# Performance work log

Measured on AMD Instinct MI355X. Metric: run time of the kernel, lower is better.

The kernel has to match this reference:

```python
import jax, jax.numpy as jnp
import numpy as np
from jax import lax

K = 4096   # input_size
N = 4096   # output_size
FP8_MAX = 448.0  # float8_e4m3fn max finite value


def setup_inputs() -> dict:
    key = jax.random.key(0)
    kx, kw, kws, kb = jax.random.split(key, 4)
    x = jax.random.normal(kx, (2, 4096, K), dtype=jnp.float32)
    # Quantized weight: sample bf16-scale weights, round to fp8_e4m3fn, store raw bits as uint8 [K, N]
    w_f32 = jax.random.normal(kw, (K, N), dtype=jnp.float32) * 8.0
    w_fp8 = jnp.clip(w_f32, -FP8_MAX, FP8_MAX).astype(jnp.float8_e4m3fn)
    qweight = lax.bitcast_convert_type(w_fp8, jnp.uint8)  # [K, N] uint8
    weight_scale = jax.random.uniform(kws, (N,), dtype=jnp.float32, minval=0.001, maxval=0.02)
    input_scale = jnp.asarray([0.01], dtype=jnp.float32)  # static activation scale [1]
    bias = jax.random.normal(kb, (N,), dtype=jnp.float32) * 0.02
    return {"x": x, "qweight": qweight, "weight_scale": weight_scale,
            "input_scale": input_scale, "bias": bias}


def reference(x, qweight, weight_scale, input_scale, bias):
    # _forward_w8a8_static: quantize activations with static scale, fp8 GEMM via
    # _scaled_mm semantics: out = (x_fp8 @ w_fp8) * input_scale * weight_scale + bias
    target_dtype = x.dtype
    x2 = x.reshape(-1, x.shape[-1]).astype(jnp.bfloat16)          # [M, K] bf16 cast as in torch path
    # static per-tensor activation quantization to fp8_e4m3fn
    xq = jnp.clip(x2.astype(jnp.float32) / input_scale[0], -FP8_MAX, FP8_MAX)
    xq = xq.astype(jnp.float8_e4m3fn).astype(jnp.float32)          # [M, K]
    w = lax.bitcast_convert_type(qweight, jnp.float8_e4m3fn).astype(jnp.float32)  # [K, N]
    acc = jnp.einsum('mk,kn->mn', xq, w)                           # fp32 accumulate
    out = acc * (input_scale[0] * weight_scale) + bias             # fused dequant scale + bias
    return out.reshape(*x.shape[:-1], N).astype(target_dtype)
```

## Files before the change

### kernel.cpp

```cpp
#include <hip/hip_runtime.h>
#include <stdint.h>

typedef float f32x4 __attribute__((ext_vector_type(4)));
typedef int   i32x4 __attribute__((ext_vector_type(4)));
typedef int   i32x8 __attribute__((ext_vector_type(8)));

__device__ __forceinline__ void gld16(const uint8_t* g, uint8_t* l) {
  __builtin_amdgcn_global_load_lds(
      (const __attribute__((address_space(1))) void*)g,
      (__attribute__((address_space(3))) void*)l, 16, 0, 0);
}

__device__ __forceinline__ float bf16_rne(float f) {
  uint32_t u = __float_as_uint(f);
  u = (u + 0x7fffu + ((u >> 16) & 1u)) & 0xffff0000u;
  return __uint_as_float(u);
}

__device__ __forceinline__ float quant_prep(float f, float s) {
  float b = bf16_rne(f);
  float v = b / s;
  return fminf(448.f, fmaxf(-448.f, v));
}

__global__ __launch_bounds__(256) void quant_x(
    const float* __restrict__ x, const float* __restrict__ isp,
    uint32_t* __restrict__ xq, int n4) {
  const float s = isp[0];
  int stride = gridDim.x * blockDim.x;
  for (int i = blockIdx.x * blockDim.x + threadIdx.x; i < n4; i += stride) {
    float4 v = ((const float4*)x)[i];
    float c0 = quant_prep(v.x, s);
    float c1 = quant_prep(v.y, s);
    float c2 = quant_prep(v.z, s);
    float c3 = quant_prep(v.w, s);
    int p = 0;
    p = __builtin_amdgcn_cvt_pk_fp8_f32(c0, c1, p, false);
    p = __builtin_amdgcn_cvt_pk_fp8_f32(c2, c3, p, true);
    xq[i] = (uint32_t)p;
  }
}

__global__ __launch_bounds__(256) void transp_w(
    const int* __restrict__ qw, uint8_t* __restrict__ wt) {
  constexpr int K = 4096, N = 4096;
  __shared__ uint8_t t[64 * 80];
  const int n0 = blockIdx.x * 64, k0 = blockIdx.y * 64;
  const int tid = threadIdx.x;
  const int r = tid >> 2, c = tid & 3;
  const int* src = qw + (size_t)(k0 + r) * N + n0 + c * 16;
  union { uint8_t b[16]; uint4 v; } o;
#pragma unroll
  for (int j = 0; j < 16; ++j) o.b[j] = (uint8_t)src[j];
  *(uint4*)(t + r * 80 + c * 16) = o.v;
  __syncthreads();
#pragma unroll
  for (int j = 0; j < 16; ++j) o.b[j] = t[(c * 16 + j) * 80 + r];
  *(uint4*)(wt + (size_t)(n0 + r) * K + k0 + c * 16) = o.v;
}

__device__ __forceinline__ i32x8 ld_frag(const uint8_t* base, int row, int g) {
  const int s = row & 7;
  const i32x4 lo = *(const i32x4*)(base + row * 128 + (((2 * g)     ^ s) * 16));
  const i32x4 hi = *(const i32x4*)(base + row * 128 + (((2 * g + 1) ^ s) * 16));
  i32x8 r;
  r[0] = lo[0]; r[1] = lo[1]; r[2] = lo[2]; r[3] = lo[3];
  r[4] = hi[0]; r[5] = hi[1]; r[6] = hi[2]; r[7] = hi[3];
  return r;
}

__global__ __launch_bounds__(256) void gemm_mxfp8(
    const uint8_t* __restrict__ xq, const uint8_t* __restrict__ wt,
    const float* __restrict__ wscale, const float* __restrict__ isp,
    const float* __restrict__ bias, float* __restrict__ out, int M) {
  constexpr int K = 4096, N = 4096, BK = 128;
  __shared__ uint8_t As[128 * BK];
  __shared__ uint8_t Bs[128 * BK];

  const int tid = threadIdx.x;
  const int l = tid & 63;
  const int w = tid >> 6;
  const int wm = w >> 1, wn = w & 1;

  const int nwg = gridDim.x;
  const int cpx = nwg >> 3;
  const int bid = blockIdx.x;
  const int swz = (bid & 7) * cpx + (bid >> 3);
  const int m0 = (swz >> 5) * 128;
  const int n0 = (swz & 31) * 128;

  f32x4 acc[4][4] = {};

  const int fr = l & 15;
  const int g  = l >> 4;

  int srow[4], scol[4];
#pragma unroll
  for (int c = 0; c < 4; ++c) {
    int u = c * 256 + tid;
    srow[c] = u >> 3;
    scol[c] = ((u & 7) ^ (srow[c] & 7)) * 16;
  }

  for (int kt = 0; kt < K; kt += BK) {
#pragma unroll
    for (int c = 0; c < 4; ++c) {
      gld16(xq + (size_t)(m0 + srow[c]) * K + kt + scol[c], As + (c * 256 + tid) * 16);
      gld16(wt + (size_t)(n0 + srow[c]) * K + kt + scol[c], Bs + (c * 256 + tid) * 16);
    }
    __syncthreads();

    i32x8 a[4], b[4];
#pragma unroll
    for (int mi = 0; mi < 4; ++mi)
      a[mi] = ld_frag(As, wm * 64 + mi * 16 + fr, g);
#pragma unroll
    for (int ni = 0; ni < 4; ++ni)
      b[ni] = ld_frag(Bs, wn * 64 + ni * 16 + fr, g);

#pragma unroll
    for (int mi = 0; mi < 4; ++mi)
#pragma unroll
      for (int ni = 0; ni < 4; ++ni)
        acc[mi][ni] = __builtin_amdgcn_mfma_scale_f32_16x16x128_f8f6f4(
            a[mi], b[ni], acc[mi][ni],
            0 , 0 ,
            0, 0x7F7F7F7Fu ,
            0, 0x7F7F7F7Fu );
    __syncthreads();
  }

  const float is = isp[0];
#pragma unroll
  for (int ni = 0; ni < 4; ++ni) {
    const int col = n0 + wn * 64 + ni * 16 + fr;
    const float sc = is * wscale[col];
    const float bb = bias[col];
#pragma unroll
    for (int mi = 0; mi < 4; ++mi) {
      const int row = m0 + wm * 64 + mi * 16 + g * 4;
      float* op = out + (size_t)row * N + col;
#pragma unroll
      for (int r = 0; r < 4; ++r)
        op[(size_t)r * N] = acc[mi][ni][r] * sc + bb;
    }
  }
}

extern "C" void kernel_launch(void* const* d_in, const int* in_sizes, int n_in,
                              void* d_out, int out_size, void* d_ws, size_t ws_size,
                              hipStream_t stream) {
  const float* x      = (const float*)d_in[0];
  const int*   qw     = (const int*)d_in[1];
  const float* wscale = (const float*)d_in[2];
  const float* isp    = (const float*)d_in[3];
  const float* bias   = (const float*)d_in[4];
  float*       out    = (float*)d_out;

  constexpr int K = 4096, N = 4096;
  const int M = in_sizes[0] / K;

  uint8_t* xq = (uint8_t*)d_ws;
  uint8_t* wt = xq + (size_t)M * K;

  quant_x<<<2048, 256, 0, stream>>>(x, isp, (uint32_t*)xq, M * K / 4);
  transp_w<<<dim3(N / 64, K / 64), 256, 0, stream>>>(qw, wt);
  gemm_mxfp8<<<(M / 128) * (N / 128), 256, 0, stream>>>(xq, wt, wscale, isp, bias, out, M);
}
```

Baseline: 446.2 us.

## Double-buffer GEMM LDS tiles and coalesce weight transpose loads

The GEMM main loop now uses two LDS buffers, issuing async global-to-LDS loads for the next K tile while MFMAs run on the current one. This hides global load latency behind compute, but doubles shared memory per block to 64KB, which may reduce occupancy. The weight transpose kernel also reads the int32 weight words as int4 vectors with coalesced row-wise access and uses a smaller padded LDS tile. The synchronisation relies on the s_waitcnt the compiler inserts before __syncthreads for the async LDS loads.

Result: no change. 440.3 us (-1.3%).

```diff
diff --git a/kernel.cpp b/kernel.cpp
--- a/kernel.cpp
+++ b/kernel.cpp
@@ -44,18 +44,23 @@
 __global__ __launch_bounds__(256) void transp_w(
     const int* __restrict__ qw, uint8_t* __restrict__ wt) {
   constexpr int K = 4096, N = 4096;
-  __shared__ uint8_t t[64 * 80];
+  __shared__ uint8_t t[64 * 68];
   const int n0 = blockIdx.x * 64, k0 = blockIdx.y * 64;
   const int tid = threadIdx.x;
+  const int lr = tid >> 4;
+  const int lc = tid & 15;
+#pragma unroll
+  for (int p = 0; p < 4; ++p) {
+    const int row = p * 16 + lr;
+    int4 v = *(const int4*)(qw + (size_t)(k0 + row) * N + n0 + lc * 4);
+    uchar4 b = make_uchar4((uint8_t)v.x, (uint8_t)v.y, (uint8_t)v.z, (uint8_t)v.w);
+    *(uchar4*)(t + row * 68 + lc * 4) = b;
+  }
+  __syncthreads();
   const int r = tid >> 2, c = tid & 3;
-  const int* src = qw + (size_t)(k0 + r) * N + n0 + c * 16;
   union { uint8_t b[16]; uint4 v; } o;
 #pragma unroll
-  for (int j = 0; j < 16; ++j) o.b[j] = (uint8_t)src[j];
-  *(uint4*)(t + r * 80 + c * 16) = o.v;
-  __syncthreads();
-#pragma unroll
-  for (int j = 0; j < 16; ++j) o.b[j] = t[(c * 16 + j) * 80 + r];
+  for (int j = 0; j < 16; ++j) o.b[j] = t[(c * 16 + j) * 68 + r];
   *(uint4*)(wt + (size_t)(n0 + r) * K + k0 + c * 16) = o.v;
 }
 
@@ -74,16 +79,17 @@
     const float* __restrict__ wscale, const float* __restrict__ isp,
     const float* __restrict__ bias, float* __restrict__ out, int M) {
   constexpr int K = 4096, N = 4096, BK = 128;
-  __shared__ uint8_t As[128 * BK];
-  __shared__ uint8_t Bs[128 * BK];
+  __shared__ uint8_t As0[128 * BK];
+  __shared__ uint8_t Bs0[128 * BK];
+  __shared__ uint8_t As1[128 * BK];
+  __shared__ uint8_t Bs1[128 * BK];
 
   const int tid = threadIdx.x;
   const int l = tid & 63;
   const int w = tid >> 6;
   const int wm = w >> 1, wn = w & 1;
 
-  const int nwg = gridDim.x;
-  const int cpx = nwg >> 3;
+  const int cpx = gridDim.x >> 3;
   const int bid = blockIdx.x;
   const int swz = (bid & 7) * cpx + (bid >> 3);
   const int m0 = (swz >> 5) * 128;
@@ -101,34 +107,43 @@
     srow[c] = u >> 3;
     scol[c] = ((u & 7) ^ (srow[c] & 7)) * 16;
   }
+  const uint8_t* abase = xq + (size_t)m0 * K;
+  const uint8_t* bbase = wt + (size_t)n0 * K;
 
-  for (int kt = 0; kt < K; kt += BK) {
-#pragma unroll
-    for (int c = 0; c < 4; ++c) {
-      gld16(xq + (size_t)(m0 + srow[c]) * K + kt + scol[c], As + (c * 256 + tid) * 16);
-      gld16(wt + (size_t)(n0 + srow[c]) * K + kt + scol[c], Bs + (c * 256 + tid) * 16);
-    }
+#define STAGE(AD, BD, KT)                                                      \
+  _Pragma("unroll")                                                            \
+  for (int c = 0; c < 4; ++c) {                                                \
+    gld16(abase + (size_t)srow[c] * K + (KT) + scol[c], (AD) + (c * 256 + tid) * 16); \
+    gld16(bbase + (size_t)srow[c] * K + (KT) + scol[c], (BD) + (c * 256 + tid) * 16); \
+  }
+
+#define COMPUTE(AS, BS)                                                        \
+  {                                                                            \
+    i32x8 a[4], b[4];                                                          \
+    _Pragma("unroll")                                                          \
+    for (int mi = 0; mi < 4; ++mi) a[mi] = ld_frag((AS), wm * 64 + mi * 16 + fr, g); \
+    _Pragma("unroll")                                                          \
+    for (int ni = 0; ni < 4; ++ni) b[ni] = ld_frag((BS), wn * 64 + ni * 16 + fr, g); \
+    _Pragma("unroll")                                                          \
+    for (int mi = 0; mi < 4; ++mi)                                             \
+      _Pragma("unroll")                                                        \
+      for (int ni = 0; ni < 4; ++ni)                                           \
+        acc[mi][ni] = __builtin_amdgcn_mfma_scale_f32_16x16x128_f8f6f4(        \
+            a[mi], b[ni], acc[mi][ni], 0, 0, 0, 0x7F7F7F7Fu, 0, 0x7F7F7F7Fu);  \
+  }
+
+  STAGE(As0, Bs0, 0);
+  __syncthreads();
+  for (int kt = 0; kt < K; kt += 2 * BK) {
+    if (kt + BK < K) { STAGE(As1, Bs1, kt + BK); }
+    COMPUTE(As0, Bs0);
     __syncthreads();
-
-    i32x8 a[4], b[4];
-#pragma unroll
-    for (int mi = 0; mi < 4; ++mi)
-      a[mi] = ld_frag(As, wm * 64 + mi * 16 + fr, g);
-#pragma unroll
-    for (int ni = 0; ni < 4; ++ni)
-      b[ni] = ld_frag(Bs, wn * 64 + ni * 16 + fr, g);
-
-#pragma unroll
-    for (int mi = 0; mi < 4; ++mi)
-#pragma unroll
-      for (int ni = 0; ni < 4; ++ni)
-        acc[mi][ni] = __builtin_amdgcn_mfma_scale_f32_16x16x128_f8f6f4(
-            a[mi], b[ni], acc[mi][ni],
-            0 , 0 ,
-            0, 0x7F7F7F7Fu ,
-            0, 0x7F7F7F7Fu );
+    if (kt + 2 * BK < K) { STAGE(As0, Bs0, kt + 2 * BK); }
+    COMPUTE(As1, Bs1);
     __syncthreads();
   }
+#undef STAGE
+#undef COMPUTE
 
   const float is = isp[0];
 #pragma unroll
```
